# Kernel tuning notes

Measured on AMD Instinct MI355X. Metric: run time of the kernel, lower is better.

## Reference

```python
import jax, jax.numpy as jnp
import numpy as np

N_NODES = 50000
N_EDGES = 1600000
IN_CH = 128
OUT_CH = 64
N_HEADS = 4


def setup_inputs() -> dict:
    key = jax.random.key(0)
    k1, k2, k3, k4, k5 = jax.random.split(key, 5)
    x_source = jax.random.normal(k1, (N_NODES, IN_CH), dtype=jnp.float32)
    edge_tgt = jax.random.randint(k2, (N_EDGES,), 0, N_NODES, dtype=jnp.int32)
    edge_src = jax.random.randint(k3, (N_EDGES,), 0, N_NODES, dtype=jnp.int32)
    edge_vals = jnp.ones((N_EDGES,), dtype=jnp.float32)
    # per-head learned params (xavier_uniform-ish scale)
    w_scale = float(np.sqrt(6.0 / (IN_CH + OUT_CH)))
    weight = jax.random.uniform(k4, (N_HEADS, IN_CH, OUT_CH), dtype=jnp.float32,
                                minval=-w_scale, maxval=w_scale)
    a_scale = float(np.sqrt(6.0 / (2 * OUT_CH)))
    att_weight = jax.random.uniform(k5, (N_HEADS, 2 * OUT_CH), dtype=jnp.float32,
                                    minval=-a_scale, maxval=a_scale)
    return {"x_source": x_source, "edge_tgt": edge_tgt, "edge_src": edge_src,
            "edge_vals": edge_vals, "weight": weight, "att_weight": att_weight}


def _can_forward(x_source, edge_tgt, edge_src, edge_vals, weight, att_weight):
    n_nodes = x_source.shape[0]
    out_ch = weight.shape[-1]
    # per-head linear transform: [N, H, O]
    x_msg = jnp.einsum('ni,hio->nho', x_source, weight)
    # gather per-edge source/target messages: [E, H, O]
    src_msg = x_msg[edge_src]
    tgt_msg = x_msg[edge_tgt]
    # attention score = cat([src, tgt]) @ att_weight, split halves: [E, H]
    aw_s = att_weight[:, :out_ch]
    aw_t = att_weight[:, out_ch:]
    e = jnp.einsum('eho,ho->eh', src_msg, aw_s) + jnp.einsum('eho,ho->eh', tgt_msg, aw_t)
    e = jax.nn.leaky_relu(e, negative_slope=0.01)  # default torch slope
    e = e * edge_vals[:, None]  # multiply by neighborhood values pre-softmax
    # sparse softmax over each target row (dim=1 of the sparse matrix)
    row_max = jax.ops.segment_max(e, edge_tgt, num_segments=n_nodes)  # [N, H]
    e_exp = jnp.exp(e - row_max[edge_tgt])
    row_sum = jax.ops.segment_sum(e_exp, edge_tgt, num_segments=n_nodes)  # [N, H]
    alpha = e_exp / row_sum[edge_tgt]  # [E, H]
    # weighted aggregate of source messages per target node: [N, H, O]
    out = jax.ops.segment_sum(alpha[:, :, None] * src_msg, edge_tgt,
                              num_segments=n_nodes)
    # concat heads -> [N, H*O]
    return out.reshape(n_nodes, -1)


def reference(x_source, edge_tgt, edge_src, edge_vals, weight, att_weight):
    return _can_forward(x_source, edge_tgt, edge_src, edge_vals, weight, att_weight)
```

## Files before the change

### kernel.cpp

```cpp
#include <hip/hip_runtime.h>
#include <hip/hip_bf16.h>
#include <math.h>

#define N_NODES 50000
#define N_EDGES 1600000
#define IN_CH   128
#define OUT_CH  64
#define N_HEADS 4
#define CH      (N_HEADS * OUT_CH)

#define NPB   64
#define BINS  782
#define CAPB  3072
#define CHUNK 8000

typedef __attribute__((ext_vector_type(8))) short bf16x8;
typedef __attribute__((ext_vector_type(4))) float f32x4;

__device__ __forceinline__ float bf16_lo(unsigned u) { return __uint_as_float(u << 16); }
__device__ __forceinline__ float bf16_hi(unsigned u) { return __uint_as_float(u & 0xffff0000u); }
__device__ __forceinline__ unsigned short f_to_bf16(float f) {
  unsigned u = __float_as_uint(f);
  u += 0x7fffu + ((u >> 16) & 1u);
  return (unsigned short)(u >> 16);
}

__global__ __launch_bounds__(256) void convert_w(
    const float* __restrict__ w, unsigned short* __restrict__ wb)
{
  int i = blockIdx.x * 256 + threadIdx.x;
  if (i >= N_HEADS * IN_CH * OUT_CH) return;
  int j = i & 7, lane = (i >> 3) & 63, ctg = (i >> 9) & 15, kc = i >> 13;
  int k = kc * 32 + (lane >> 4) * 8 + j;
  int n = ctg * 16 + (lane & 15);
  int h = n >> 6, o = n & 63;
  wb[i] = f_to_bf16(w[(h * IN_CH + k) * OUT_CH + o]);
}

__global__ __launch_bounds__(256) void init_cursors(int* __restrict__ gcur)
{
  int b = blockIdx.x * 256 + threadIdx.x;
  if (b < BINS) gcur[b] = b * CAPB;
}

__global__ __launch_bounds__(256) void gemm_mfma(
    const float* __restrict__ x, const unsigned short* __restrict__ wb,
    const float* __restrict__ aw,
    unsigned short* __restrict__ xmsg, float* __restrict__ sbuf, float* __restrict__ tbuf)
{
  __shared__ __align__(16) unsigned short tlds[4][32][128];

  const int lane = threadIdx.x & 63;
  const int wv   = threadIdx.x >> 6;
  const int q    = lane >> 4;
  const int l16  = lane & 15;
  const int rowbase = blockIdx.x * 64 + (wv >> 1) * 32;
  const int chalf   = wv & 1;

  bf16x8 afrag[2][4];
  #pragma unroll
  for (int s = 0; s < 2; ++s) {
    int r = rowbase + s * 16 + l16;
    r = min(r, N_NODES - 1);
    const float* xp = x + (size_t)r * IN_CH + q * 8;
    #pragma unroll
    for (int kc = 0; kc < 4; ++kc) {
      f32x4 lo = *(const f32x4*)(xp + kc * 32);
      f32x4 hi = *(const f32x4*)(xp + kc * 32 + 4);
      bf16x8 a;
      a[0] = (short)f_to_bf16(lo[0]); a[1] = (short)f_to_bf16(lo[1]);
      a[2] = (short)f_to_bf16(lo[2]); a[3] = (short)f_to_bf16(lo[3]);
      a[4] = (short)f_to_bf16(hi[0]); a[5] = (short)f_to_bf16(hi[1]);
      a[6] = (short)f_to_bf16(hi[2]); a[7] = (short)f_to_bf16(hi[3]);
      afrag[s][kc] = a;
    }
  }

  f32x4 acc[2][8];
  #pragma unroll
  for (int s = 0; s < 2; ++s)
    #pragma unroll
    for (int ct = 0; ct < 8; ++ct)
      acc[s][ct] = (f32x4){0.f, 0.f, 0.f, 0.f};

  #pragma unroll
  for (int kc = 0; kc < 4; ++kc) {
    #pragma unroll
    for (int ct = 0; ct < 8; ++ct) {
      const int ctg = chalf * 8 + ct;
      bf16x8 b = *(const bf16x8*)(wb + ((size_t)(kc * 16 + ctg) * 64 + lane) * 8);
      acc[0][ct] = __builtin_amdgcn_mfma_f32_16x16x32_bf16(afrag[0][kc], b, acc[0][ct], 0, 0, 0);
      acc[1][ct] = __builtin_amdgcn_mfma_f32_16x16x32_bf16(afrag[1][kc], b, acc[1][ct], 0, 0, 0);
    }
  }

  #pragma unroll
  for (int s = 0; s < 2; ++s)
    #pragma unroll
    for (int ct = 0; ct < 8; ++ct)
      #pragma unroll
      for (int reg = 0; reg < 4; ++reg)
        tlds[wv][s * 16 + q * 4 + reg][ct * 16 + l16] = f_to_bf16(acc[s][ct][reg]);

  #pragma unroll
  for (int s = 0; s < 2; ++s) {
    float ps[2][4] = {{0,0,0,0},{0,0,0,0}};
    float pt[2][4] = {{0,0,0,0},{0,0,0,0}};
    #pragma unroll
    for (int ct = 0; ct < 8; ++ct) {
      int col = chalf * 128 + ct * 16 + l16;
      int h = col >> 6;
      float as_ = aw[h * 128 + (col & 63)];
      float at_ = aw[h * 128 + 64 + (col & 63)];
      int hp = ct >> 2;
      #pragma unroll
      for (int reg = 0; reg < 4; ++reg) {
        float v = acc[s][ct][reg];
        ps[hp][reg] += v * as_;
        pt[hp][reg] += v * at_;
      }
    }
    #pragma unroll
    for (int hp = 0; hp < 2; ++hp)
      #pragma unroll
      for (int reg = 0; reg < 4; ++reg)
        #pragma unroll
        for (int off = 1; off < 16; off <<= 1) {
          ps[hp][reg] += __shfl_xor(ps[hp][reg], off);
          pt[hp][reg] += __shfl_xor(pt[hp][reg], off);
        }
    const int rowq = rowbase + s * 16 + q * 4;
    if (l16 == 0) {
      #pragma unroll
      for (int reg = 0; reg < 4; ++reg) {
        int r = rowq + reg;
        if (r < N_NODES) {
          #pragma unroll
          for (int hp = 0; hp < 2; ++hp) {
            sbuf[r * 4 + chalf * 2 + hp] = ps[hp][reg];
            tbuf[r * 4 + chalf * 2 + hp] = pt[hp][reg];
          }
        }
      }
    }
  }

  __syncthreads();

  const int seg  = lane & 31;
  const int half = lane >> 5;
  #pragma unroll
  for (int r2 = 0; r2 < 16; ++r2) {
    int row = r2 * 2 + half;
    int gr = rowbase + row;
    if (gr < N_NODES) {
      ushort4 vv = *(const ushort4*)&tlds[wv][row][seg * 4];
      *(ushort4*)(xmsg + (size_t)gr * CH + chalf * 128 + seg * 4) = vv;
    }
  }
}

__global__ __launch_bounds__(256) void bin_scatter(
    const int* __restrict__ etgt, const int* __restrict__ esrc,
    const float* __restrict__ eval, int* __restrict__ gcur, int2* __restrict__ binned)
{
  __shared__ int lhist[BINS];
  __shared__ int lbase[BINS];
  __shared__ unsigned short stg[CHUNK];

  const int tid = threadIdx.x;
  const int e0 = blockIdx.x * CHUNK;
  const int n = min(CHUNK, N_EDGES - e0);

  for (int b = tid; b < BINS; b += 256) lhist[b] = 0;
  __syncthreads();

  for (int i = tid; i < n; i += 256) {
    int t = etgt[e0 + i];
    stg[i] = (unsigned short)t;
    atomicAdd(&lhist[t >> 6], 1);
  }
  __syncthreads();

  for (int b = tid; b < BINS; b += 256) {
    int c = lhist[b];
    lbase[b] = c ? atomicAdd(&gcur[b], c) : 0;
    lhist[b] = 0;
  }
  __syncthreads();

  for (int i = tid; i < n; i += 256) {
    int t = (int)stg[i];
    int b = t >> 6;
    int r = atomicAdd(&lhist[b], 1);
    int pos = lbase[b] + r;
    if (pos < (b + 1) * CAPB) {
      int pack = esrc[e0 + i] | ((t & 63) << 16);
      binned[pos] = make_int2(pack, __float_as_int(eval[e0 + i]));
    }
  }
}

__global__ __launch_bounds__(256) void build_csr(
    const int* __restrict__ gcur, const int2* __restrict__ binned,
    int2* __restrict__ csr, int* __restrict__ deg, int* __restrict__ rowstart)
{
  __shared__ int nh[NPB];
  __shared__ int npre[NPB];
  __shared__ __align__(16) int2 stg[CAPB];

  const int tid = threadIdx.x;
  const int b = blockIdx.x;
  const int base = b * CAPB;
  const int cnt = min(gcur[b] - base, CAPB);

  if (tid < NPB) nh[tid] = 0;
  __syncthreads();

  for (int i = tid; i < cnt; i += 256) {
    int2 e = binned[base + i];
    stg[i] = e;
    atomicAdd(&nh[(e.x >> 16) & 63], 1);
  }
  __syncthreads();

  if (tid < 64) {
    int v = nh[tid];
    int sc = v;
    #pragma unroll
    for (int off = 1; off < 64; off <<= 1) {
      int u = __shfl_up(sc, off);
      if (tid >= off) sc += u;
    }
    npre[tid] = sc - v;
    int node = b * NPB + tid;
    if (node < N_NODES) { deg[node] = v; rowstart[node] = base + sc - v; }
    nh[tid] = 0;
  }
  __syncthreads();

  for (int i = tid; i < cnt; i += 256) {
    int2 e = stg[i];
    int tl = (e.x >> 16) & 63;
    int r = atomicAdd(&nh[tl], 1);
    csr[base + npre[tl] + r] = e;
  }
}

__global__ __launch_bounds__(256) void aggregate_kernel(
    const int* __restrict__ deg, const int* __restrict__ rowstart,
    const int2* __restrict__ csr,
    const float* __restrict__ sbuf, const float* __restrict__ tbuf,
    const unsigned short* __restrict__ xmsg, float* __restrict__ out)
{
  const int lane = threadIdx.x & 63;
  const int wave = threadIdx.x >> 6;
  const int n = blockIdx.x * 4 + wave;
  if (n >= N_NODES) return;

  __shared__ __align__(16) float p_lds[4][64][4];
  __shared__ int s_lds[4][64];

  const int d = deg[n];
  const int rs0 = rowstart[n];
  const int seg  = lane & 31;
  const int half = lane >> 5;
  const int hh4  = seg >> 3;

  float4 tn4 = *(const float4*)(tbuf + (size_t)n * 4);
  float tn[4] = {tn4.x, tn4.y, tn4.z, tn4.w};

  float m[4]    = {-INFINITY, -INFINITY, -INFINITY, -INFINITY};
  float psum[4] = {0.f, 0.f, 0.f, 0.f};
  float acc[8]  = {0.f, 0.f, 0.f, 0.f, 0.f, 0.f, 0.f, 0.f};

  for (int base = 0; base < d; base += 64) {
    const int cnt = min(64, d - base);
    const bool act = lane < cnt;

    float sc[4] = {-INFINITY, -INFINITY, -INFINITY, -INFINITY};
    int s = 0;
    if (act) {
      int2 ev = csr[(size_t)rs0 + base + lane];
      s = ev.x & 0xffff;
      float v = __int_as_float(ev.y);
      float4 sv4 = *(const float4*)(sbuf + (size_t)s * 4);
      float svv[4] = {sv4.x, sv4.y, sv4.z, sv4.w};
      #pragma unroll
      for (int hh = 0; hh < 4; ++hh) {
        float t = svv[hh] + tn[hh];
        t = (t > 0.f) ? t : 0.01f * t;
        sc[hh] = t * v;
      }
    }

    float bm[4] = {sc[0], sc[1], sc[2], sc[3]};
    #pragma unroll
    for (int hh = 0; hh < 4; ++hh)
      #pragma unroll
      for (int off = 32; off; off >>= 1)
        bm[hh] = fmaxf(bm[hh], __shfl_xor(bm[hh], off));

    float p[4];
    #pragma unroll
    for (int hh = 0; hh < 4; ++hh) {
      float nm = fmaxf(m[hh], bm[hh]);
      float r = (m[hh] == -INFINITY) ? 0.f : __expf(m[hh] - nm);
      psum[hh] *= r;
      if (hh == hh4) {
        #pragma unroll
        for (int j = 0; j < 8; ++j) acc[j] *= r;
      }
      m[hh] = nm;
      p[hh] = act ? __expf(sc[hh] - nm) : 0.f;
      psum[hh] += p[hh];
    }

    if (act) {
      s_lds[wave][lane] = s;
      *(float4*)(&p_lds[wave][lane][0]) = make_float4(p[0], p[1], p[2], p[3]);
    }
    __builtin_amdgcn_wave_barrier();

    int k = 0;
    for (; k + 8 <= cnt; k += 8) {
      int sA = s_lds[wave][k + 0 + half];
      int sB = s_lds[wave][k + 2 + half];
      int sC = s_lds[wave][k + 4 + half];
      int sD = s_lds[wave][k + 6 + half];
      uint4 rA = *(const uint4*)(xmsg + (size_t)sA * CH + seg * 8);
      uint4 rB = *(const uint4*)(xmsg + (size_t)sB * CH + seg * 8);
      uint4 rC = *(const uint4*)(xmsg + (size_t)sC * CH + seg * 8);
      uint4 rD = *(const uint4*)(xmsg + (size_t)sD * CH + seg * 8);
      float qA = p_lds[wave][k + 0 + half][hh4];
      float qB = p_lds[wave][k + 2 + half][hh4];
      float qC = p_lds[wave][k + 4 + half][hh4];
      float qD = p_lds[wave][k + 6 + half][hh4];
      acc[0] = fmaf(qA, bf16_lo(rA.x), acc[0]); acc[1] = fmaf(qA, bf16_hi(rA.x), acc[1]);
      acc[2] = fmaf(qA, bf16_lo(rA.y), acc[2]); acc[3] = fmaf(qA, bf16_hi(rA.y), acc[3]);
      acc[4] = fmaf(qA, bf16_lo(rA.z), acc[4]); acc[5] = fmaf(qA, bf16_hi(rA.z), acc[5]);
      acc[6] = fmaf(qA, bf16_lo(rA.w), acc[6]); acc[7] = fmaf(qA, bf16_hi(rA.w), acc[7]);
      acc[0] = fmaf(qB, bf16_lo(rB.x), acc[0]); acc[1] = fmaf(qB, bf16_hi(rB.x), acc[1]);
      acc[2] = fmaf(qB, bf16_lo(rB.y), acc[2]); acc[3] = fmaf(qB, bf16_hi(rB.y), acc[3]);
      acc[4] = fmaf(qB, bf16_lo(rB.z), acc[4]); acc[5] = fmaf(qB, bf16_hi(rB.z), acc[5]);
      acc[6] = fmaf(qB, bf16_lo(rB.w), acc[6]); acc[7] = fmaf(qB, bf16_hi(rB.w), acc[7]);
      acc[0] = fmaf(qC, bf16_lo(rC.x), acc[0]); acc[1] = fmaf(qC, bf16_hi(rC.x), acc[1]);
      acc[2] = fmaf(qC, bf16_lo(rC.y), acc[2]); acc[3] = fmaf(qC, bf16_hi(rC.y), acc[3]);
      acc[4] = fmaf(qC, bf16_lo(rC.z), acc[4]); acc[5] = fmaf(qC, bf16_hi(rC.z), acc[5]);
      acc[6] = fmaf(qC, bf16_lo(rC.w), acc[6]); acc[7] = fmaf(qC, bf16_hi(rC.w), acc[7]);
      acc[0] = fmaf(qD, bf16_lo(rD.x), acc[0]); acc[1] = fmaf(qD, bf16_hi(rD.x), acc[1]);
      acc[2] = fmaf(qD, bf16_lo(rD.y), acc[2]); acc[3] = fmaf(qD, bf16_hi(rD.y), acc[3]);
      acc[4] = fmaf(qD, bf16_lo(rD.z), acc[4]); acc[5] = fmaf(qD, bf16_hi(rD.z), acc[5]);
      acc[6] = fmaf(qD, bf16_lo(rD.w), acc[6]); acc[7] = fmaf(qD, bf16_hi(rD.w), acc[7]);
    }
    for (; k < cnt; k += 2) {
      int e = k + half;
      if (e < cnt) {
        int sA = s_lds[wave][e];
        uint4 rA = *(const uint4*)(xmsg + (size_t)sA * CH + seg * 8);
        float qA = p_lds[wave][e][hh4];
        acc[0] = fmaf(qA, bf16_lo(rA.x), acc[0]); acc[1] = fmaf(qA, bf16_hi(rA.x), acc[1]);
        acc[2] = fmaf(qA, bf16_lo(rA.y), acc[2]); acc[3] = fmaf(qA, bf16_hi(rA.y), acc[3]);
        acc[4] = fmaf(qA, bf16_lo(rA.z), acc[4]); acc[5] = fmaf(qA, bf16_hi(rA.z), acc[5]);
        acc[6] = fmaf(qA, bf16_lo(rA.w), acc[6]); acc[7] = fmaf(qA, bf16_hi(rA.w), acc[7]);
      }
    }
    __builtin_amdgcn_wave_barrier();
  }

  #pragma unroll
  for (int j = 0; j < 8; ++j) acc[j] += __shfl_xor(acc[j], 32);
  #pragma unroll
  for (int hh = 0; hh < 4; ++hh)
    #pragma unroll
    for (int off = 32; off; off >>= 1)
      psum[hh] += __shfl_xor(psum[hh], off);

  float rs = psum[hh4];
  float inv = (rs > 0.f) ? 1.0f / rs : 0.f;
  const int o = half * 4;
  float4 o4 = make_float4(acc[o+0]*inv, acc[o+1]*inv, acc[o+2]*inv, acc[o+3]*inv);
  *(float4*)(out + (size_t)n * CH + seg * 8 + half * 4) = o4;
}

extern "C" void kernel_launch(void* const* d_in, const int* in_sizes, int n_in,
                              void* d_out, int out_size, void* d_ws, size_t ws_size,
                              hipStream_t stream) {
  const float* x    = (const float*)d_in[0];
  const int*   etgt = (const int*)  d_in[1];
  const int*   esrc = (const int*)  d_in[2];
  const float* evl  = (const float*)d_in[3];
  const float* w    = (const float*)d_in[4];
  const float* aw   = (const float*)d_in[5];
  float* out = (float*)d_out;

  char* ws = (char*)d_ws;
  unsigned short* wb   = (unsigned short*)(ws);
  unsigned short* xmsg = (unsigned short*)(ws + 65536);
  float* sbuf     = (float*)(ws + 25665536);
  float* tbuf     = (float*)(ws + 26465536);
  int*   gcur     = (int*)  (ws + 27265536);
  int*   deg      = (int*)  (ws + 27269632);
  int*   rowstart = (int*)  (ws + 27470336);
  int2*  binned   = (int2*) (ws + 27671040);
  int2*  csr      = (int2*) (ws + 46889472);

  init_cursors<<<4, 256, 0, stream>>>(gcur);
  convert_w<<<128, 256, 0, stream>>>(w, wb);
  gemm_mfma<<<(N_NODES + 63) / 64, 256, 0, stream>>>(x, wb, aw, xmsg, sbuf, tbuf);
  bin_scatter<<<(N_EDGES + CHUNK - 1) / CHUNK, 256, 0, stream>>>(etgt, esrc, evl, gcur, binned);
  build_csr<<<BINS, 256, 0, stream>>>(gcur, binned, csr, deg, rowstart);
  aggregate_kernel<<<(N_NODES + 3) / 4, 256, 0, stream>>>(deg, rowstart, csr,
                                                          sbuf, tbuf, xmsg, out);
}
```

Before: 288.9 us.

## Fuse GEMM with edge binning and CSR build with aggregation

Merges init_cursors into the weight conversion, runs the edge bin-scatter and the MFMA GEMM as disjoint block ranges of one launch, and fuses the per-bin CSR sort into the aggregation kernel. The sorted edges now stay in LDS, so the global csr/deg/rowstart buffers and their round trip go away, and the kernel count drops from six to three. In exchange the aggregation kernel uses large LDS (about 24KB for the sorted edges plus staging) with 512-thread blocks, one block per 64-node bin. That may limit occupancy and leave load imbalance across bins.

```diff
diff --git a/kernel.cpp b/kernel.cpp
--- a/kernel.cpp
+++ b/kernel.cpp
@@ -13,6 +13,8 @@
 #define BINS  782
 #define CAPB  3072
 #define CHUNK 8000
+#define NSCAT 200
+#define GEMMB 782
 
 typedef __attribute__((ext_vector_type(8))) short bf16x8;
 typedef __attribute__((ext_vector_type(4))) float f32x4;
@@ -25,10 +27,11 @@
   return (unsigned short)(u >> 16);
 }
 
-__global__ __launch_bounds__(256) void convert_w(
-    const float* __restrict__ w, unsigned short* __restrict__ wb)
+__global__ __launch_bounds__(256) void convert_w_init(
+    const float* __restrict__ w, unsigned short* __restrict__ wb, int* __restrict__ gcur)
 {
   int i = blockIdx.x * 256 + threadIdx.x;
+  if (i < BINS) gcur[i] = i * CAPB;
   if (i >= N_HEADS * IN_CH * OUT_CH) return;
   int j = i & 7, lane = (i >> 3) & 63, ctg = (i >> 9) & 15, kc = i >> 13;
   int k = kc * 32 + (lane >> 4) * 8 + j;
@@ -37,24 +40,62 @@
   wb[i] = f_to_bf16(w[(h * IN_CH + k) * OUT_CH + o]);
 }
 
-__global__ __launch_bounds__(256) void init_cursors(int* __restrict__ gcur)
-{
-  int b = blockIdx.x * 256 + threadIdx.x;
-  if (b < BINS) gcur[b] = b * CAPB;
-}
-
-__global__ __launch_bounds__(256) void gemm_mfma(
+__global__ __launch_bounds__(256) void gemm_scatter(
     const float* __restrict__ x, const unsigned short* __restrict__ wb,
     const float* __restrict__ aw,
-    unsigned short* __restrict__ xmsg, float* __restrict__ sbuf, float* __restrict__ tbuf)
+    unsigned short* __restrict__ xmsg, float* __restrict__ sbuf, float* __restrict__ tbuf,
+    const int* __restrict__ etgt, const int* __restrict__ esrc,
+    const float* __restrict__ eval, int* __restrict__ gcur, int2* __restrict__ binned)
 {
-  __shared__ __align__(16) unsigned short tlds[4][32][128];
-
+  __shared__ __align__(16) char smem[32768];
+
+  if (blockIdx.x < NSCAT) {
+    int* lhist = (int*)smem;
+    int* lbase = lhist + BINS;
+    unsigned short* stg = (unsigned short*)(lbase + BINS);
+
+    const int tid = threadIdx.x;
+    const int e0 = blockIdx.x * CHUNK;
+    const int n = min(CHUNK, N_EDGES - e0);
+
+    for (int b = tid; b < BINS; b += 256) lhist[b] = 0;
+    __syncthreads();
+
+    for (int i = tid; i < n; i += 256) {
+      int t = etgt[e0 + i];
+      stg[i] = (unsigned short)t;
+      atomicAdd(&lhist[t >> 6], 1);
+    }
+    __syncthreads();
+
+    for (int b = tid; b < BINS; b += 256) {
+      int c = lhist[b];
+      lbase[b] = c ? atomicAdd(&gcur[b], c) : 0;
+      lhist[b] = 0;
+    }
+    __syncthreads();
+
+    for (int i = tid; i < n; i += 256) {
+      int t = (int)stg[i];
+      int b = t >> 6;
+      int r = atomicAdd(&lhist[b], 1);
+      int pos = lbase[b] + r;
+      if (pos < (b + 1) * CAPB) {
+        int pack = esrc[e0 + i] | ((t & 63) << 16);
+        binned[pos] = make_int2(pack, __float_as_int(eval[e0 + i]));
+      }
+    }
+    return;
+  }
+
+  unsigned short (*tlds)[32][128] = (unsigned short (*)[32][128])smem;
+
+  const int gbid = blockIdx.x - NSCAT;
   const int lane = threadIdx.x & 63;
   const int wv   = threadIdx.x >> 6;
   const int q    = lane >> 4;
   const int l16  = lane & 15;
-  const int rowbase = blockIdx.x * 64 + (wv >> 1) * 32;
+  const int rowbase = gbid * 64 + (wv >> 1) * 32;
   const int chalf   = wv & 1;
 
   bf16x8 afrag[2][4];
@@ -160,54 +201,17 @@
   }
 }
 
-__global__ __launch_bounds__(256) void bin_scatter(
-    const int* __restrict__ etgt, const int* __restrict__ esrc,
-    const float* __restrict__ eval, int* __restrict__ gcur, int2* __restrict__ binned)
-{
-  __shared__ int lhist[BINS];
-  __shared__ int lbase[BINS];
-  __shared__ unsigned short stg[CHUNK];
-
-  const int tid = threadIdx.x;
-  const int e0 = blockIdx.x * CHUNK;
-  const int n = min(CHUNK, N_EDGES - e0);
-
-  for (int b = tid; b < BINS; b += 256) lhist[b] = 0;
-  __syncthreads();
-
-  for (int i = tid; i < n; i += 256) {
-    int t = etgt[e0 + i];
-    stg[i] = (unsigned short)t;
-    atomicAdd(&lhist[t >> 6], 1);
-  }
-  __syncthreads();
-
-  for (int b = tid; b < BINS; b += 256) {
-    int c = lhist[b];
-    lbase[b] = c ? atomicAdd(&gcur[b], c) : 0;
-    lhist[b] = 0;
-  }
-  __syncthreads();
-
-  for (int i = tid; i < n; i += 256) {
-    int t = (int)stg[i];
-    int b = t >> 6;
-    int r = atomicAdd(&lhist[b], 1);
-    int pos = lbase[b] + r;
-    if (pos < (b + 1) * CAPB) {
-      int pack = esrc[e0 + i] | ((t & 63) << 16);
-      binned[pos] = make_int2(pack, __float_as_int(eval[e0 + i]));
-    }
-  }
-}
-
-__global__ __launch_bounds__(256) void build_csr(
+__global__ __launch_bounds__(512, 8) void csr_aggregate(
     const int* __restrict__ gcur, const int2* __restrict__ binned,
-    int2* __restrict__ csr, int* __restrict__ deg, int* __restrict__ rowstart)
+    const float* __restrict__ sbuf, const float* __restrict__ tbuf,
+    const unsigned short* __restrict__ xmsg, float* __restrict__ out)
 {
   __shared__ int nh[NPB];
-  __shared__ int npre[NPB];
-  __shared__ __align__(16) int2 stg[CAPB];
+  __shared__ int start_l[NPB];
+  __shared__ int deg_l[NPB];
+  __shared__ __align__(16) int2 sorted[CAPB];
+  __shared__ int s_stage[8][64];
+  __shared__ __align__(16) float p_stage[8][64][4];
 
   const int tid = threadIdx.x;
   const int b = blockIdx.x;
@@ -217,11 +221,8 @@
   if (tid < NPB) nh[tid] = 0;
   __syncthreads();
 
-  for (int i = tid; i < cnt; i += 256) {
-    int2 e = binned[base + i];
-    stg[i] = e;
-    atomicAdd(&nh[(e.x >> 16) & 63], 1);
-  }
+  for (int i = tid; i < cnt; i += 512)
+    atomicAdd(&nh[(binned[base + i].x >> 16) & 63], 1);
   __syncthreads();
 
   if (tid < 64) {
@@ -232,155 +233,148 @@
       int u = __shfl_up(sc, off);
       if (tid >= off) sc += u;
     }
-    npre[tid] = sc - v;
-    int node = b * NPB + tid;
-    if (node < N_NODES) { deg[node] = v; rowstart[node] = base + sc - v; }
+    start_l[tid] = sc - v;
+    deg_l[tid] = v;
     nh[tid] = 0;
   }
   __syncthreads();
 
-  for (int i = tid; i < cnt; i += 256) {
-    int2 e = stg[i];
+  for (int i = tid; i < cnt; i += 512) {
+    int2 e = binned[base + i];
     int tl = (e.x >> 16) & 63;
     int r = atomicAdd(&nh[tl], 1);
-    csr[base + npre[tl] + r] = e;
-  }
-}
-
-__global__ __launch_bounds__(256) void aggregate_kernel(
-    const int* __restrict__ deg, const int* __restrict__ rowstart,
-    const int2* __restrict__ csr,
-    const float* __restrict__ sbuf, const float* __restrict__ tbuf,
-    const unsigned short* __restrict__ xmsg, float* __restrict__ out)
-{
-  const int lane = threadIdx.x & 63;
-  const int wave = threadIdx.x >> 6;
-  const int n = blockIdx.x * 4 + wave;
-  if (n >= N_NODES) return;
-
-  __shared__ __align__(16) float p_lds[4][64][4];
-  __shared__ int s_lds[4][64];
-
-  const int d = deg[n];
-  const int rs0 = rowstart[n];
+    sorted[start_l[tl] + r] = e;
+  }
+  __syncthreads();
+
+  const int lane = tid & 63;
+  const int wave = tid >> 6;
   const int seg  = lane & 31;
   const int half = lane >> 5;
   const int hh4  = seg >> 3;
 
-  float4 tn4 = *(const float4*)(tbuf + (size_t)n * 4);
-  float tn[4] = {tn4.x, tn4.y, tn4.z, tn4.w};
-
-  float m[4]    = {-INFINITY, -INFINITY, -INFINITY, -INFINITY};
-  float psum[4] = {0.f, 0.f, 0.f, 0.f};
-  float acc[8]  = {0.f, 0.f, 0.f, 0.f, 0.f, 0.f, 0.f, 0.f};
-
-  for (int base = 0; base < d; base += 64) {
-    const int cnt = min(64, d - base);
-    const bool act = lane < cnt;
-
-    float sc[4] = {-INFINITY, -INFINITY, -INFINITY, -INFINITY};
-    int s = 0;
-    if (act) {
-      int2 ev = csr[(size_t)rs0 + base + lane];
-      s = ev.x & 0xffff;
-      float v = __int_as_float(ev.y);
-      float4 sv4 = *(const float4*)(sbuf + (size_t)s * 4);
-      float svv[4] = {sv4.x, sv4.y, sv4.z, sv4.w};
+  for (int ni = wave; ni < NPB; ni += 8) {
+    const int n = b * NPB + ni;
+    if (n >= N_NODES) break;
+
+    const int d   = deg_l[ni];
+    const int rs0 = start_l[ni];
+
+    float4 tn4 = *(const float4*)(tbuf + (size_t)n * 4);
+    float tn[4] = {tn4.x, tn4.y, tn4.z, tn4.w};
+
+    float m[4]    = {-INFINITY, -INFINITY, -INFINITY, -INFINITY};
+    float psum[4] = {0.f, 0.f, 0.f, 0.f};
+    float acc[8]  = {0.f, 0.f, 0.f, 0.f, 0.f, 0.f, 0.f, 0.f};
+
+    for (int base2 = 0; base2 < d; base2 += 64) {
+      const int cnt2 = min(64, d - base2);
+      const bool act = lane < cnt2;
+
+      float sc[4] = {-INFINITY, -INFINITY, -INFINITY, -INFINITY};
+      int s = 0;
+      if (act) {
+        int2 ev = sorted[rs0 + base2 + lane];
+        s = ev.x & 0xffff;
+        float v = __int_as_float(ev.y);
+        float4 sv4 = *(const float4*)(sbuf + (size_t)s * 4);
+        float svv[4] = {sv4.x, sv4.y, sv4.z, sv4.w};
+        #pragma unroll
+        for (int hh = 0; hh < 4; ++hh) {
+          float t = svv[hh] + tn[hh];
+          t = (t > 0.f) ? t : 0.01f * t;
+          sc[hh] = t * v;
+        }
+      }
+
+      float bm[4] = {sc[0], sc[1], sc[2], sc[3]};
+      #pragma unroll
+      for (int hh = 0; hh < 4; ++hh)
+        #pragma unroll
+        for (int off = 32; off; off >>= 1)
+          bm[hh] = fmaxf(bm[hh], __shfl_xor(bm[hh], off));
+
+      float p[4];
       #pragma unroll
       for (int hh = 0; hh < 4; ++hh) {
-        float t = svv[hh] + tn[hh];
-        t = (t > 0.f) ? t : 0.01f * t;
-        sc[hh] = t * v;
-      }
-    }
-
-    float bm[4] = {sc[0], sc[1], sc[2], sc[3]};
-    #pragma unroll
-    for (int hh = 0; hh < 4; ++hh)
-      #pragma unroll
-      for (int off = 32; off; off >>= 1)
-        bm[hh] = fmaxf(bm[hh], __shfl_xor(bm[hh], off));
-
-    float p[4];
-    #pragma unroll
-    for (int hh = 0; hh < 4; ++hh) {
-      float nm = fmaxf(m[hh], bm[hh]);
-      float r = (m[hh] == -INFINITY) ? 0.f : __expf(m[hh] - nm);
-      psum[hh] *= r;
-      if (hh == hh4) {
-        #pragma unroll
-        for (int j = 0; j < 8; ++j) acc[j] *= r;
-      }
-      m[hh] = nm;
-      p[hh] = act ? __expf(sc[hh] - nm) : 0.f;
-      psum[hh] += p[hh];
-    }
-
-    if (act) {
-      s_lds[wave][lane] = s;
-      *(float4*)(&p_lds[wave][lane][0]) = make_float4(p[0], p[1], p[2], p[3]);
-    }
-    __builtin_amdgcn_wave_barrier();
-
-    int k = 0;
-    for (; k + 8 <= cnt; k += 8) {
-      int sA = s_lds[wave][k + 0 + half];
-      int sB = s_lds[wave][k + 2 + half];
-      int sC = s_lds[wave][k + 4 + half];
-      int sD = s_lds[wave][k + 6 + half];
-      uint4 rA = *(const uint4*)(xmsg + (size_t)sA * CH + seg * 8);
-      uint4 rB = *(const uint4*)(xmsg + (size_t)sB * CH + seg * 8);
-      uint4 rC = *(const uint4*)(xmsg + (size_t)sC * CH + seg * 8);
-      uint4 rD = *(const uint4*)(xmsg + (size_t)sD * CH + seg * 8);
-      float qA = p_lds[wave][k + 0 + half][hh4];
-      float qB = p_lds[wave][k + 2 + half][hh4];
-      float qC = p_lds[wave][k + 4 + half][hh4];
-      float qD = p_lds[wave][k + 6 + half][hh4];
-      acc[0] = fmaf(qA, bf16_lo(rA.x), acc[0]); acc[1] = fmaf(qA, bf16_hi(rA.x), acc[1]);
-      acc[2] = fmaf(qA, bf16_lo(rA.y), acc[2]); acc[3] = fmaf(qA, bf16_hi(rA.y), acc[3]);
-      acc[4] = fmaf(qA, bf16_lo(rA.z), acc[4]); acc[5] = fmaf(qA, bf16_hi(rA.z), acc[5]);
-      acc[6] = fmaf(qA, bf16_lo(rA.w), acc[6]); acc[7] = fmaf(qA, bf16_hi(rA.w), acc[7]);
-      acc[0] = fmaf(qB, bf16_lo(rB.x), acc[0]); acc[1] = fmaf(qB, bf16_hi(rB.x), acc[1]);
-      acc[2] = fmaf(qB, bf16_lo(rB.y), acc[2]); acc[3] = fmaf(qB, bf16_hi(rB.y), acc[3]);
-      acc[4] = fmaf(qB, bf16_lo(rB.z), acc[4]); acc[5] = fmaf(qB, bf16_hi(rB.z), acc[5]);
-      acc[6] = fmaf(qB, bf16_lo(rB.w), acc[6]); acc[7] = fmaf(qB, bf16_hi(rB.w), acc[7]);
-      acc[0] = fmaf(qC, bf16_lo(rC.x), acc[0]); acc[1] = fmaf(qC, bf16_hi(rC.x), acc[1]);
-      acc[2] = fmaf(qC, bf16_lo(rC.y), acc[2]); acc[3] = fmaf(qC, bf16_hi(rC.y), acc[3]);
-      acc[4] = fmaf(qC, bf16_lo(rC.z), acc[4]); acc[5] = fmaf(qC, bf16_hi(rC.z), acc[5]);
-      acc[6] = fmaf(qC, bf16_lo(rC.w), acc[6]); acc[7] = fmaf(qC, bf16_hi(rC.w), acc[7]);
-      acc[0] = fmaf(qD, bf16_lo(rD.x), acc[0]); acc[1] = fmaf(qD, bf16_hi(rD.x), acc[1]);
-      acc[2] = fmaf(qD, bf16_lo(rD.y), acc[2]); acc[3] = fmaf(qD, bf16_hi(rD.y), acc[3]);
-      acc[4] = fmaf(qD, bf16_lo(rD.z), acc[4]); acc[5] = fmaf(qD, bf16_hi(rD.z), acc[5]);
-      acc[6] = fmaf(qD, bf16_lo(rD.w), acc[6]); acc[7] = fmaf(qD, bf16_hi(rD.w), acc[7]);
-    }
-    for (; k < cnt; k += 2) {
-      int e = k + half;
-      if (e < cnt) {
-        int sA = s_lds[wave][e];
+        float nm = fmaxf(m[hh], bm[hh]);
+        float r = (m[hh] == -INFINITY) ? 0.f : __expf(m[hh] - nm);
+        psum[hh] *= r;
+        if (hh == hh4) {
+          #pragma unroll
+          for (int j = 0; j < 8; ++j) acc[j] *= r;
+        }
+        m[hh] = nm;
+        p[hh] = act ? __expf(sc[hh] - nm) : 0.f;
+        psum[hh] += p[hh];
+      }
+
+      if (act) {
+        s_stage[wave][lane] = s;
+        *(float4*)(&p_stage[wave][lane][0]) = make_float4(p[0], p[1], p[2], p[3]);
+      }
+      __builtin_amdgcn_wave_barrier();
+
+      int k = 0;
+      for (; k + 8 <= cnt2; k += 8) {
+        int sA = s_stage[wave][k + 0 + half];
+        int sB = s_stage[wave][k + 2 + half];
+        int sC = s_stage[wave][k + 4 + half];
+        int sD = s_stage[wave][k + 6 + half];
         uint4 rA = *(const uint4*)(xmsg + (size_t)sA * CH + seg * 8);
-        float qA = p_lds[wave][e][hh4];
+        uint4 rB = *(const uint4*)(xmsg + (size_t)sB * CH + seg * 8);
+        uint4 rC = *(const uint4*)(xmsg + (size_t)sC * CH + seg * 8);
+        uint4 rD = *(const uint4*)(xmsg + (size_t)sD * CH + seg * 8);
+        float qA = p_stage[wave][k + 0 + half][hh4];
+        float qB = p_stage[wave][k + 2 + half][hh4];
+        float qC = p_stage[wave][k + 4 + half][hh4];
+        float qD = p_stage[wave][k + 6 + half][hh4];
         acc[0] = fmaf(qA, bf16_lo(rA.x), acc[0]); acc[1] = fmaf(qA, bf16_hi(rA.x), acc[1]);
         acc[2] = fmaf(qA, bf16_lo(rA.y), acc[2]); acc[3] = fmaf(qA, bf16_hi(rA.y), acc[3]);
         acc[4] = fmaf(qA, bf16_lo(rA.z), acc[4]); acc[5] = fmaf(qA, bf16_hi(rA.z), acc[5]);
         acc[6] = fmaf(qA, bf16_lo(rA.w), acc[6]); acc[7] = fmaf(qA, bf16_hi(rA.w), acc[7]);
-      }
-    }
-    __builtin_amdgcn_wave_barrier();
-  }
-
-  #pragma unroll
-  for (int j = 0; j < 8; ++j) acc[j] += __shfl_xor(acc[j], 32);
-  #pragma unroll
-  for (int hh = 0; hh < 4; ++hh)
-    #pragma unroll
-    for (int off = 32; off; off >>= 1)
-      psum[hh] += __shfl_xor(psum[hh], off);
-
-  float rs = psum[hh4];
-  float inv = (rs > 0.f) ? 1.0f / rs : 0.f;
-  const int o = half * 4;
-  float4 o4 = make_float4(acc[o+0]*inv, acc[o+1]*inv, acc[o+2]*inv, acc[o+3]*inv);
-  *(float4*)(out + (size_t)n * CH + seg * 8 + half * 4) = o4;
+        acc[0] = fmaf(qB, bf16_lo(rB.x), acc[0]); acc[1] = fmaf(qB, bf16_hi(rB.x), acc[1]);
+        acc[2] = fmaf(qB, bf16_lo(rB.y), acc[2]); acc[3] = fmaf(qB, bf16_hi(rB.y), acc[3]);
+        acc[4] = fmaf(qB, bf16_lo(rB.z), acc[4]); acc[5] = fmaf(qB, bf16_hi(rB.z), acc[5]);
+        acc[6] = fmaf(qB, bf16_lo(rB.w), acc[6]); acc[7] = fmaf(qB, bf16_hi(rB.w), acc[7]);
+        acc[0] = fmaf(qC, bf16_lo(rC.x), acc[0]); acc[1] = fmaf(qC, bf16_hi(rC.x), acc[1]);
+        acc[2] = fmaf(qC, bf16_lo(rC.y), acc[2]); acc[3] = fmaf(qC, bf16_hi(rC.y), acc[3]);
+        acc[4] = fmaf(qC, bf16_lo(rC.z), acc[4]); acc[5] = fmaf(qC, bf16_hi(rC.z), acc[5]);
+        acc[6] = fmaf(qC, bf16_lo(rC.w), acc[6]); acc[7] = fmaf(qC, bf16_hi(rC.w), acc[7]);
+        acc[0] = fmaf(qD, bf16_lo(rD.x), acc[0]); acc[1] = fmaf(qD, bf16_hi(rD.x), acc[1]);
+        acc[2] = fmaf(qD, bf16_lo(rD.y), acc[2]); acc[3] = fmaf(qD, bf16_hi(rD.y), acc[3]);
+        acc[4] = fmaf(qD, bf16_lo(rD.z), acc[4]); acc[5] = fmaf(qD, bf16_hi(rD.z), acc[5]);
+        acc[6] = fmaf(qD, bf16_lo(rD.w), acc[6]); acc[7] = fmaf(qD, bf16_hi(rD.w), acc[7]);
+      }
+      for (; k < cnt2; k += 2) {
+        int e = k + half;
+        if (e < cnt2) {
+          int sA = s_stage[wave][e];
+          uint4 rA = *(const uint4*)(xmsg + (size_t)sA * CH + seg * 8);
+          float qA = p_stage[wave][e][hh4];
+          acc[0] = fmaf(qA, bf16_lo(rA.x), acc[0]); acc[1] = fmaf(qA, bf16_hi(rA.x), acc[1]);
+          acc[2] = fmaf(qA, bf16_lo(rA.y), acc[2]); acc[3] = fmaf(qA, bf16_hi(rA.y), acc[3]);
+          acc[4] = fmaf(qA, bf16_lo(rA.z), acc[4]); acc[5] = fmaf(qA, bf16_hi(rA.z), acc[5]);
+          acc[6] = fmaf(qA, bf16_lo(rA.w), acc[6]); acc[7] = fmaf(qA, bf16_hi(rA.w), acc[7]);
+        }
+      }
+      __builtin_amdgcn_wave_barrier();
+    }
+
+    #pragma unroll
+    for (int j = 0; j < 8; ++j) acc[j] += __shfl_xor(acc[j], 32);
+    #pragma unroll
+    for (int hh = 0; hh < 4; ++hh)
+      #pragma unroll
+      for (int off = 32; off; off >>= 1)
+        psum[hh] += __shfl_xor(psum[hh], off);
+
+    float rs = psum[hh4];
+    float inv = (rs > 0.f) ? 1.0f / rs : 0.f;
+    const int o = half * 4;
+    float4 o4 = make_float4(acc[o+0]*inv, acc[o+1]*inv, acc[o+2]*inv, acc[o+3]*inv);
+    *(float4*)(out + (size_t)n * CH + seg * 8 + half * 4) = o4;
+  }
 }
 
 extern "C" void kernel_launch(void* const* d_in, const int* in_sizes, int n_in,
@@ -400,16 +394,10 @@
   float* sbuf     = (float*)(ws + 25665536);
   float* tbuf     = (float*)(ws + 26465536);
   int*   gcur     = (int*)  (ws + 27265536);
-  int*   deg      = (int*)  (ws + 27269632);
-  int*   rowstart = (int*)  (ws + 27470336);
   int2*  binned   = (int2*) (ws + 27671040);
-  int2*  csr      = (int2*) (ws + 46889472);
-
-  init_cursors<<<4, 256, 0, stream>>>(gcur);
-  convert_w<<<128, 256, 0, stream>>>(w, wb);
-  gemm_mfma<<<(N_NODES + 63) / 64, 256, 0, stream>>>(x, wb, aw, xmsg, sbuf, tbuf);
-  bin_scatter<<<(N_EDGES + CHUNK - 1) / CHUNK, 256, 0, stream>>>(etgt, esrc, evl, gcur, binned);
-  build_csr<<<BINS, 256, 0, stream>>>(gcur, binned, csr, deg, rowstart);
-  aggregate_kernel<<<(N_NODES + 3) / 4, 256, 0, stream>>>(deg, rowstart, csr,
-                                                          sbuf, tbuf, xmsg, out);
+
+  convert_w_init<<<128, 256, 0, stream>>>(w, wb, gcur);
+  gemm_scatter<<<NSCAT + GEMMB, 256, 0, stream>>>(x, wb, aw, xmsg, sbuf, tbuf,
+                                                  etgt, esrc, evl, gcur, binned);
+  csr_aggregate<<<BINS, 512, 0, stream>>>(gcur, binned, sbuf, tbuf, xmsg, out);
 }
```

After: 418.3 us. +44.8%, slower.

## Fuse GEMM and edge binning into one heterogeneous launch, merge init kernels

Applied to the files above, without the earlier changes.

Combines the node-feature GEMM and the edge bin-scatter into a single kernel whose first blocks do scattering and remaining blocks do the MFMA GEMM, so the two independent stages run concurrently on the GPU. Cursor initialization is folded into the weight-conversion kernel, removing a launch. The scatter chunk size is reduced to spread edges over more blocks, which increases global atomic traffic on the bin cursors. Shared memory is unified into a 32KB buffer sized for the larger user, which may lower occupancy for the GEMM blocks.

```diff
diff --git a/kernel.cpp b/kernel.cpp
--- a/kernel.cpp
+++ b/kernel.cpp
@@ -12,7 +12,9 @@
 #define NPB   64
 #define BINS  782
 #define CAPB  3072
-#define CHUNK 8000
+#define CHUNK 3200
+#define NSCAT 500
+#define GEMMB 782
 
 typedef __attribute__((ext_vector_type(8))) short bf16x8;
 typedef __attribute__((ext_vector_type(4))) float f32x4;
@@ -25,10 +27,11 @@
   return (unsigned short)(u >> 16);
 }
 
-__global__ __launch_bounds__(256) void convert_w(
-    const float* __restrict__ w, unsigned short* __restrict__ wb)
+__global__ __launch_bounds__(256) void convert_w_init(
+    const float* __restrict__ w, unsigned short* __restrict__ wb, int* __restrict__ gcur)
 {
   int i = blockIdx.x * 256 + threadIdx.x;
+  if (i < BINS) gcur[i] = i * CAPB;
   if (i >= N_HEADS * IN_CH * OUT_CH) return;
   int j = i & 7, lane = (i >> 3) & 63, ctg = (i >> 9) & 15, kc = i >> 13;
   int k = kc * 32 + (lane >> 4) * 8 + j;
@@ -37,24 +40,62 @@
   wb[i] = f_to_bf16(w[(h * IN_CH + k) * OUT_CH + o]);
 }
 
-__global__ __launch_bounds__(256) void init_cursors(int* __restrict__ gcur)
-{
-  int b = blockIdx.x * 256 + threadIdx.x;
-  if (b < BINS) gcur[b] = b * CAPB;
-}
-
-__global__ __launch_bounds__(256) void gemm_mfma(
+__global__ __launch_bounds__(256) void gemm_scatter(
     const float* __restrict__ x, const unsigned short* __restrict__ wb,
     const float* __restrict__ aw,
-    unsigned short* __restrict__ xmsg, float* __restrict__ sbuf, float* __restrict__ tbuf)
+    unsigned short* __restrict__ xmsg, float* __restrict__ sbuf, float* __restrict__ tbuf,
+    const int* __restrict__ etgt, const int* __restrict__ esrc,
+    const float* __restrict__ eval, int* __restrict__ gcur, int2* __restrict__ binned)
 {
-  __shared__ __align__(16) unsigned short tlds[4][32][128];
-
+  __shared__ __align__(16) char smem[32768];
+
+  if (blockIdx.x < NSCAT) {
+    int* lhist = (int*)smem;
+    int* lbase = lhist + BINS;
+    unsigned short* stg = (unsigned short*)(lbase + BINS);
+
+    const int tid = threadIdx.x;
+    const int e0 = blockIdx.x * CHUNK;
+    const int n = min(CHUNK, N_EDGES - e0);
+
+    for (int b = tid; b < BINS; b += 256) lhist[b] = 0;
+    __syncthreads();
+
+    for (int i = tid; i < n; i += 256) {
+      int t = etgt[e0 + i];
+      stg[i] = (unsigned short)t;
+      atomicAdd(&lhist[t >> 6], 1);
+    }
+    __syncthreads();
+
+    for (int b = tid; b < BINS; b += 256) {
+      int c = lhist[b];
+      lbase[b] = c ? atomicAdd(&gcur[b], c) : 0;
+      lhist[b] = 0;
+    }
+    __syncthreads();
+
+    for (int i = tid; i < n; i += 256) {
+      int t = (int)stg[i];
+      int b = t >> 6;
+      int r = atomicAdd(&lhist[b], 1);
+      int pos = lbase[b] + r;
+      if (pos < (b + 1) * CAPB) {
+        int pack = esrc[e0 + i] | ((t & 63) << 16);
+        binned[pos] = make_int2(pack, __float_as_int(eval[e0 + i]));
+      }
+    }
+    return;
+  }
+
+  unsigned short (*tlds)[32][128] = (unsigned short (*)[32][128])smem;
+
+  const int gbid = blockIdx.x - NSCAT;
   const int lane = threadIdx.x & 63;
   const int wv   = threadIdx.x >> 6;
   const int q    = lane >> 4;
   const int l16  = lane & 15;
-  const int rowbase = blockIdx.x * 64 + (wv >> 1) * 32;
+  const int rowbase = gbid * 64 + (wv >> 1) * 32;
   const int chalf   = wv & 1;
 
   bf16x8 afrag[2][4];
@@ -156,47 +197,6 @@
     if (gr < N_NODES) {
       ushort4 vv = *(const ushort4*)&tlds[wv][row][seg * 4];
       *(ushort4*)(xmsg + (size_t)gr * CH + chalf * 128 + seg * 4) = vv;
-    }
-  }
-}
-
-__global__ __launch_bounds__(256) void bin_scatter(
-    const int* __restrict__ etgt, const int* __restrict__ esrc,
-    const float* __restrict__ eval, int* __restrict__ gcur, int2* __restrict__ binned)
-{
-  __shared__ int lhist[BINS];
-  __shared__ int lbase[BINS];
-  __shared__ unsigned short stg[CHUNK];
-
-  const int tid = threadIdx.x;
-  const int e0 = blockIdx.x * CHUNK;
-  const int n = min(CHUNK, N_EDGES - e0);
-
-  for (int b = tid; b < BINS; b += 256) lhist[b] = 0;
-  __syncthreads();
-
-  for (int i = tid; i < n; i += 256) {
-    int t = etgt[e0 + i];
-    stg[i] = (unsigned short)t;
-    atomicAdd(&lhist[t >> 6], 1);
-  }
-  __syncthreads();
-
-  for (int b = tid; b < BINS; b += 256) {
-    int c = lhist[b];
-    lbase[b] = c ? atomicAdd(&gcur[b], c) : 0;
-    lhist[b] = 0;
-  }
-  __syncthreads();
-
-  for (int i = tid; i < n; i += 256) {
-    int t = (int)stg[i];
-    int b = t >> 6;
-    int r = atomicAdd(&lhist[b], 1);
-    int pos = lbase[b] + r;
-    if (pos < (b + 1) * CAPB) {
-      int pack = esrc[e0 + i] | ((t & 63) << 16);
-      binned[pos] = make_int2(pack, __float_as_int(eval[e0 + i]));
     }
   }
 }
@@ -405,10 +405,9 @@
   int2*  binned   = (int2*) (ws + 27671040);
   int2*  csr      = (int2*) (ws + 46889472);
 
-  init_cursors<<<4, 256, 0, stream>>>(gcur);
-  convert_w<<<128, 256, 0, stream>>>(w, wb);
-  gemm_mfma<<<(N_NODES + 63) / 64, 256, 0, stream>>>(x, wb, aw, xmsg, sbuf, tbuf);
-  bin_scatter<<<(N_EDGES + CHUNK - 1) / CHUNK, 256, 0, stream>>>(etgt, esrc, evl, gcur, binned);
+  convert_w_init<<<128, 256, 0, stream>>>(w, wb, gcur);
+  gemm_scatter<<<NSCAT + GEMMB, 256, 0, stream>>>(x, wb, aw, xmsg, sbuf, tbuf,
+                                                  etgt, esrc, evl, gcur, binned);
   build_csr<<<BINS, 256, 0, stream>>>(gcur, binned, csr, deg, rowstart);
   aggregate_kernel<<<(N_NODES + 3) / 4, 256, 0, stream>>>(deg, rowstart, csr,
                                                           sbuf, tbuf, xmsg, out);
```

Result: faster. 276.4 us (-4.3%).
